# Performance work log

Hardware: AMD Instinct MI355X
Metric: run time of the kernel (lower is better)

The kernel has to match this reference:

```python
import jax, jax.numpy as jnp
import numpy as np
import math

B, H, S, D = 2, 16, 2048, 128

def setup_inputs() -> dict:
    key = jax.random.key(0)
    kq, kk, kv = jax.random.split(key, 3)
    return {
        "query": jax.random.normal(kq, (B, H, S, D), dtype=jnp.float32),
        "key": jax.random.normal(kk, (B, H, S, D), dtype=jnp.float32),
        "value": jax.random.normal(kv, (B, H, S, D), dtype=jnp.float32),
        "mask": jnp.ones((1, 1, S, S), dtype=jnp.bool_),
    }

def reference(query, key, value, mask):
    # scale_factor=None -> 1/sqrt(head_dim), as in standard SDPA
    head_dim = query.shape[-1]
    scale = 1.0 / math.sqrt(head_dim)
    # [B,H,Sq,Sk] attention scores
    scores = jnp.einsum("bhqd,bhkd->bhqk", query, key) * scale
    neg_inf = jnp.finfo(scores.dtype).min
    scores = jnp.where(mask, scores, neg_inf)
    attn = jax.nn.softmax(scores, axis=-1)  # dropout p=0.0 -> identity
    return jnp.einsum("bhqk,bhkd->bhqd", attn, value)
```

## Files before the change

kernel.cpp:

```cpp
#include <hip/hip_runtime.h>
#include <cstdint>

using short8  = __attribute__((ext_vector_type(8))) short;
using short2v = __attribute__((ext_vector_type(2))) short;
using f32x16  = __attribute__((ext_vector_type(16))) float;
using float4v = __attribute__((ext_vector_type(4))) float;
using int4v   = __attribute__((ext_vector_type(4))) int;

constexpr int Bc = 2, Hc = 16, Sc = 2048, Dc = 128;
constexpr int NW = 8, QBLK = 256;
constexpr int KVS = 128;
constexpr int NT = Sc / KVS;
constexpr float SCALE_LOG2E = 0.08838834764831845f * 1.4426950408889634f;

__device__ __forceinline__ short f2bf(float f) {
  union { float f; uint32_t u; } v; v.f = f;
  uint32_t u = v.u;
  uint32_t r = (u + 0x7FFFu + ((u >> 16) & 1u)) >> 16;
  return (short)r;
}

__device__ __forceinline__ uint32_t cvtpk(float lo, float hi) {
  uint32_t r;
  asm("v_cvt_pk_bf16_f32 %0, %1, %2" : "=v"(r) : "v"(lo), "v"(hi));
  return r;
}

#define GLOAD_LDS16(g, l)                                                     \
  __builtin_amdgcn_global_load_lds(                                           \
      (const __attribute__((address_space(1))) void*)(g),                     \
      (__attribute__((address_space(3))) void*)(l), 16, 0, 0)

__global__ __launch_bounds__(256)
void prep_v_kernel(const float* __restrict__ V, ushort* __restrict__ Vt) {
  __shared__ short T[64 * 66];
  const int bh = blockIdx.y;
  const int st = blockIdx.x & 31, dt = blockIdx.x >> 5;
  const int s0 = st * 64, d0 = dt * 64;
  const float* Vb = V + (size_t)bh * Sc * Dc;
  ushort* Vtb = Vt + (size_t)bh * Dc * Sc;
#pragma unroll
  for (int i = 0; i < 4; ++i) {
    int idx = threadIdx.x + i * 256;
    int r = idx >> 4, c4 = (idx & 15) * 4;
    float4v v = *(const float4v*)&Vb[(size_t)(s0 + r) * Dc + d0 + c4];
    short2v lo, hi;
    lo[0] = f2bf(v[0]); lo[1] = f2bf(v[1]);
    hi[0] = f2bf(v[2]); hi[1] = f2bf(v[3]);
    *(short2v*)&T[r * 66 + c4]     = lo;
    *(short2v*)&T[r * 66 + c4 + 2] = hi;
  }
  __syncthreads();
#pragma unroll
  for (int i = 0; i < 2; ++i) {
    int idx = threadIdx.x + i * 256;
    int dr = idx >> 3, c8 = (idx & 7) * 8;
    short8 o;
#pragma unroll
    for (int j = 0; j < 8; ++j) o[j] = T[(c8 + j) * 66 + dr];
    *(short8*)&Vtb[(size_t)(d0 + dr) * Sc + s0 + c8] = o;
  }
}

__global__ __launch_bounds__(512, 2)
void sdpa_fwd_kernel(const float* __restrict__ Q, const float* __restrict__ Kf,
                     const ushort* __restrict__ Vt, float* __restrict__ O) {
  __shared__ __align__(16) short Kl[2][KVS * Dc];
  __shared__ __align__(16) short Vl[2][Dc * KVS];

  const int tid  = threadIdx.x;
  const int w    = tid >> 6;
  const int lane = tid & 63;
  const int l31  = lane & 31;
  const int hi   = lane >> 5;

  const int bh = blockIdx.x & 31;
  const int qt = blockIdx.x >> 5;
  const size_t base = (size_t)bh * Sc * Dc;
  const float* Qb = Q + base;
  const float* KfB = Kf + base;
  const ushort* VtB = Vt + base;

  const int qrow = qt * QBLK + w * 32 + l31;

  short8 qf[8];
#pragma unroll
  for (int c = 0; c < 8; ++c) {
    const float* src = Qb + (size_t)qrow * Dc + c * 16 + hi * 8;
    float4v a = *(const float4v*)src;
    float4v b = *(const float4v*)(src + 4);
    short8 r;
    r[0] = f2bf(a[0] * SCALE_LOG2E); r[1] = f2bf(a[1] * SCALE_LOG2E);
    r[2] = f2bf(a[2] * SCALE_LOG2E); r[3] = f2bf(a[3] * SCALE_LOG2E);
    r[4] = f2bf(b[0] * SCALE_LOG2E); r[5] = f2bf(b[1] * SCALE_LOG2E);
    r[6] = f2bf(b[2] * SCALE_LOG2E); r[7] = f2bf(b[3] * SCALE_LOG2E);
    qf[c] = r;
  }

  int offK[4], kdst[4], offV[4], vldsOff[4];
#pragma unroll
  for (int j = 0; j < 4; ++j) {
    int row = w * 16 + j * 4 + (lane >> 4);
    offK[j] = row * Dc + (((lane & 15) ^ (row & 15)) * 8);
    kdst[j] = (w * 16 + j * 4) * Dc + lane * 8;
    int d = w * 16 + j * 4 + (lane >> 4);
    offV[j] = d * Sc + (((lane & 15) ^ (d & 15)) * 8);
    vldsOff[j] = (w * 16 + j * 4) * KVS;
  }

  float4v krA[4], krB[4];
  auto LOADK = [&](int kv0) {
#pragma unroll
    for (int j = 0; j < 4; ++j) {
      const float* s = KfB + (size_t)kv0 * Dc + offK[j];
      krA[j] = *(const float4v*)s;
      krB[j] = *(const float4v*)(s + 4);
    }
  };
  auto WRITEK = [&](int buf) {
#pragma unroll
    for (int j = 0; j < 4; ++j) {
      int4v kw;
      kw[0] = (int)cvtpk(krA[j][0], krA[j][1]);
      kw[1] = (int)cvtpk(krA[j][2], krA[j][3]);
      kw[2] = (int)cvtpk(krB[j][0], krB[j][1]);
      kw[3] = (int)cvtpk(krB[j][2], krB[j][3]);
      *(int4v*)&Kl[buf][kdst[j]] = kw;
    }
  };
  auto STAGEV = [&](int buf, int kv0) {
#pragma unroll
    for (int j = 0; j < 4; ++j)
      GLOAD_LDS16(VtB + kv0 + offV[j], &Vl[buf][vldsOff[j]]);
  };

  f32x16 acc[4];
#pragma unroll
  for (int i = 0; i < 4; ++i)
#pragma unroll
    for (int r = 0; r < 16; ++r) acc[i][r] = 0.f;
  float m_run = -1e30f, l_run = 0.f;

  LOADK(0);
  WRITEK(0);
  STAGEV(0, 0);
  LOADK(KVS);
  int cur = 0;

  for (int it = 0; it < NT; ++it) {
    __syncthreads();
    if (it + 1 < NT) { WRITEK(cur ^ 1); STAGEV(cur ^ 1, (it + 1) * KVS); }
    if (it + 2 < NT) LOADK((it + 2) * KVS);

#pragma unroll
    for (int sub = 0; sub < 2; ++sub) {
      f32x16 st0, st1;
#pragma unroll
      for (int r = 0; r < 16; ++r) { st0[r] = 0.f; st1[r] = 0.f; }
      __builtin_amdgcn_s_setprio(1);
#pragma unroll
      for (int c = 0; c < 8; ++c) {
        int e0 = ((sub * 64 + l31) * Dc + c * 16 + hi * 8) ^ ((l31 & 15) << 3);
        int e1 = ((sub * 64 + 32 + l31) * Dc + c * 16 + hi * 8) ^ ((l31 & 15) << 3);
        short8 kf0 = *(const short8*)&Kl[cur][e0];
        short8 kf1 = *(const short8*)&Kl[cur][e1];
        st0 = __builtin_amdgcn_mfma_f32_32x32x16_bf16(kf0, qf[c], st0, 0, 0, 0);
        st1 = __builtin_amdgcn_mfma_f32_32x32x16_bf16(kf1, qf[c], st1, 0, 0, 0);
      }
      __builtin_amdgcn_s_setprio(0);

      float t0 = st0[0], t1 = st0[1], t2 = st0[2], t3 = st0[3];
#pragma unroll
      for (int r = 4; r < 16; r += 4) {
        t0 = fmaxf(t0, st0[r]);     t1 = fmaxf(t1, st0[r + 1]);
        t2 = fmaxf(t2, st0[r + 2]); t3 = fmaxf(t3, st0[r + 3]);
      }
#pragma unroll
      for (int r = 0; r < 16; r += 4) {
        t0 = fmaxf(t0, st1[r]);     t1 = fmaxf(t1, st1[r + 1]);
        t2 = fmaxf(t2, st1[r + 2]); t3 = fmaxf(t3, st1[r + 3]);
      }
      float tmax = fmaxf(fmaxf(t0, t1), fmaxf(t2, t3));
      tmax = fmaxf(tmax, __shfl_xor(tmax, 32));

      if (!__all(tmax <= m_run + 8.0f)) {
        float m_new = fmaxf(m_run, tmax);
        float alpha = __builtin_amdgcn_exp2f(m_run - m_new);
        l_run *= alpha;
#pragma unroll
        for (int i = 0; i < 4; ++i)
#pragma unroll
          for (int r = 0; r < 16; ++r) acc[i][r] *= alpha;
        m_run = m_new;
      }

      float ps0 = 0.f, ps1 = 0.f, ps2 = 0.f, ps3 = 0.f;
#pragma unroll
      for (int r = 0; r < 16; r += 4) {
        float p0 = __builtin_amdgcn_exp2f(st0[r]     - m_run);
        float p1 = __builtin_amdgcn_exp2f(st0[r + 1] - m_run);
        float p2 = __builtin_amdgcn_exp2f(st0[r + 2] - m_run);
        float p3 = __builtin_amdgcn_exp2f(st0[r + 3] - m_run);
        st0[r] = p0; st0[r + 1] = p1; st0[r + 2] = p2; st0[r + 3] = p3;
        ps0 += p0; ps1 += p1; ps2 += p2; ps3 += p3;
      }
#pragma unroll
      for (int r = 0; r < 16; r += 4) {
        float p0 = __builtin_amdgcn_exp2f(st1[r]     - m_run);
        float p1 = __builtin_amdgcn_exp2f(st1[r + 1] - m_run);
        float p2 = __builtin_amdgcn_exp2f(st1[r + 2] - m_run);
        float p3 = __builtin_amdgcn_exp2f(st1[r + 3] - m_run);
        st1[r] = p0; st1[r + 1] = p1; st1[r + 2] = p2; st1[r + 3] = p3;
        ps0 += p0; ps1 += p1; ps2 += p2; ps3 += p3;
      }
      float psum = (ps0 + ps1) + (ps2 + ps3);
      psum += __shfl_xor(psum, 32);
      l_run += psum;

      short8 pf[4];
#pragma unroll
      for (int kc = 0; kc < 4; ++kc) {
        const f32x16& stq = (kc < 2) ? st0 : st1;
        const int g0 = (2 * kc) & 3, g1 = (2 * kc + 1) & 3;
        uint32_t a0 = cvtpk(stq[4 * g0 + 0], stq[4 * g0 + 1]);
        uint32_t b0 = cvtpk(stq[4 * g1 + 0], stq[4 * g1 + 1]);
        asm volatile("v_permlane32_swap_b32 %0, %1" : "+v"(a0), "+v"(b0));
        uint32_t a1 = cvtpk(stq[4 * g0 + 2], stq[4 * g0 + 3]);
        uint32_t b1 = cvtpk(stq[4 * g1 + 2], stq[4 * g1 + 3]);
        asm volatile("v_permlane32_swap_b32 %0, %1" : "+v"(a1), "+v"(b1));
        int4v wv; wv[0] = (int)a0; wv[1] = (int)a1; wv[2] = (int)b0; wv[3] = (int)b1;
        union { int4v i; short8 s; } u; u.i = wv;
        pf[kc] = u.s;
      }

      __builtin_amdgcn_s_setprio(1);
#pragma unroll
      for (int kc = 0; kc < 4; ++kc) {
#pragma unroll
        for (int dt = 0; dt < 4; ++dt) {
          int d = dt * 32 + l31;
          int elem = (d * KVS + sub * 64 + kc * 16 + hi * 8) ^ ((l31 & 15) << 3);
          short8 vf = *(const short8*)&Vl[cur][elem];
          acc[dt] = __builtin_amdgcn_mfma_f32_32x32x16_bf16(vf, pf[kc], acc[dt], 0, 0, 0);
        }
      }
      __builtin_amdgcn_s_setprio(0);
    }
    cur ^= 1;
  }

  const float inv_l = 1.0f / l_run;
  float* Ob = O + base + (size_t)qrow * Dc;
#pragma unroll
  for (int dt = 0; dt < 4; ++dt)
#pragma unroll
    for (int g = 0; g < 4; ++g) {
      float4v o;
      o[0] = acc[dt][4 * g + 0] * inv_l; o[1] = acc[dt][4 * g + 1] * inv_l;
      o[2] = acc[dt][4 * g + 2] * inv_l; o[3] = acc[dt][4 * g + 3] * inv_l;
      *(float4v*)&Ob[dt * 32 + 8 * g + 4 * hi] = o;
    }
}

extern "C" void kernel_launch(void* const* d_in, const int* in_sizes, int n_in,
                              void* d_out, int out_size, void* d_ws, size_t ws_size,
                              hipStream_t stream) {
  const float* Q = (const float*)d_in[0];
  const float* K = (const float*)d_in[1];
  const float* V = (const float*)d_in[2];
  float* O = (float*)d_out;

  ushort* Vt = (ushort*)d_ws;

  prep_v_kernel<<<dim3(64, Bc * Hc), dim3(256), 0, stream>>>(V, Vt);

  sdpa_fwd_kernel<<<dim3((Sc / QBLK) * Bc * Hc), dim3(512), 0, stream>>>(Q, K, Vt, O);
}
```

Measured before the change: 94.44 us.

## Fuse V bf16 conversion and transpose into attention kernel, drop prep kernel

Removes the separate kernel that converted V to bf16 and transposed it into workspace. Each attention block now loads fp32 V rows into registers, converts them, and scatters them transposed into swizzled LDS alongside the K pipeline. This removes a launch and a workspace round trip. In exchange it reads fp32 V once per query tile, adds many scalar 16-bit LDS stores per tile, and raises register pressure.

```diff
diff --git a/kernel.cpp b/kernel.cpp
--- a/kernel.cpp
+++ b/kernel.cpp
@@ -2,7 +2,6 @@
 #include <cstdint>
 
 using short8  = __attribute__((ext_vector_type(8))) short;
-using short2v = __attribute__((ext_vector_type(2))) short;
 using f32x16  = __attribute__((ext_vector_type(16))) float;
 using float4v = __attribute__((ext_vector_type(4))) float;
 using int4v   = __attribute__((ext_vector_type(4))) int;
@@ -26,45 +25,9 @@
   return r;
 }
 
-#define GLOAD_LDS16(g, l)                                                     \
-  __builtin_amdgcn_global_load_lds(                                           \
-      (const __attribute__((address_space(1))) void*)(g),                     \
-      (__attribute__((address_space(3))) void*)(l), 16, 0, 0)
-
-__global__ __launch_bounds__(256)
-void prep_v_kernel(const float* __restrict__ V, ushort* __restrict__ Vt) {
-  __shared__ short T[64 * 66];
-  const int bh = blockIdx.y;
-  const int st = blockIdx.x & 31, dt = blockIdx.x >> 5;
-  const int s0 = st * 64, d0 = dt * 64;
-  const float* Vb = V + (size_t)bh * Sc * Dc;
-  ushort* Vtb = Vt + (size_t)bh * Dc * Sc;
-#pragma unroll
-  for (int i = 0; i < 4; ++i) {
-    int idx = threadIdx.x + i * 256;
-    int r = idx >> 4, c4 = (idx & 15) * 4;
-    float4v v = *(const float4v*)&Vb[(size_t)(s0 + r) * Dc + d0 + c4];
-    short2v lo, hi;
-    lo[0] = f2bf(v[0]); lo[1] = f2bf(v[1]);
-    hi[0] = f2bf(v[2]); hi[1] = f2bf(v[3]);
-    *(short2v*)&T[r * 66 + c4]     = lo;
-    *(short2v*)&T[r * 66 + c4 + 2] = hi;
-  }
-  __syncthreads();
-#pragma unroll
-  for (int i = 0; i < 2; ++i) {
-    int idx = threadIdx.x + i * 256;
-    int dr = idx >> 3, c8 = (idx & 7) * 8;
-    short8 o;
-#pragma unroll
-    for (int j = 0; j < 8; ++j) o[j] = T[(c8 + j) * 66 + dr];
-    *(short8*)&Vtb[(size_t)(d0 + dr) * Sc + s0 + c8] = o;
-  }
-}
-
 __global__ __launch_bounds__(512, 2)
 void sdpa_fwd_kernel(const float* __restrict__ Q, const float* __restrict__ Kf,
-                     const ushort* __restrict__ Vt, float* __restrict__ O) {
+                     const float* __restrict__ Vf, float* __restrict__ O) {
   __shared__ __align__(16) short Kl[2][KVS * Dc];
   __shared__ __align__(16) short Vl[2][Dc * KVS];
 
@@ -79,7 +42,7 @@
   const size_t base = (size_t)bh * Sc * Dc;
   const float* Qb = Q + base;
   const float* KfB = Kf + base;
-  const ushort* VtB = Vt + base;
+  const float* VfB = Vf + base;
 
   const int qrow = qt * QBLK + w * 32 + l31;
 
@@ -97,15 +60,12 @@
     qf[c] = r;
   }
 
-  int offK[4], kdst[4], offV[4], vldsOff[4];
+  int offK[4], kdst[4];
 #pragma unroll
   for (int j = 0; j < 4; ++j) {
     int row = w * 16 + j * 4 + (lane >> 4);
     offK[j] = row * Dc + (((lane & 15) ^ (row & 15)) * 8);
     kdst[j] = (w * 16 + j * 4) * Dc + lane * 8;
-    int d = w * 16 + j * 4 + (lane >> 4);
-    offV[j] = d * Sc + (((lane & 15) ^ (d & 15)) * 8);
-    vldsOff[j] = (w * 16 + j * 4) * KVS;
   }
 
   float4v krA[4], krB[4];
@@ -128,10 +88,30 @@
       *(int4v*)&Kl[buf][kdst[j]] = kw;
     }
   };
-  auto STAGEV = [&](int buf, int kv0) {
-#pragma unroll
-    for (int j = 0; j < 4; ++j)
-      GLOAD_LDS16(VtB + kv0 + offV[j], &Vl[buf][vldsOff[j]]);
+
+  const int kvp = lane & 15, dp = lane >> 4;
+  const int kvv = w * 16 + kvp;
+  float4v vrA[4], vrB[4];
+  auto LOADV = [&](int kv0) {
+#pragma unroll
+    for (int j = 0; j < 4; ++j) {
+      const float* s = VfB + (size_t)(kv0 + kvv) * Dc + j * 32 + dp * 8;
+      vrA[j] = *(const float4v*)s;
+      vrB[j] = *(const float4v*)(s + 4);
+    }
+  };
+  auto WRITEV = [&](int buf) {
+    short* vl = &Vl[buf][0];
+#pragma unroll
+    for (int j = 0; j < 4; ++j) {
+#pragma unroll
+      for (int e = 0; e < 8; ++e) {
+        int dd = j * 32 + dp * 8 + e;
+        int flat = (dd * KVS + kvv) ^ ((dd & 15) << 3);
+        float x = (e < 4) ? vrA[j][e & 3] : vrB[j][e & 3];
+        vl[flat] = f2bf(x);
+      }
+    }
   };
 
   f32x16 acc[4];
@@ -141,16 +121,15 @@
     for (int r = 0; r < 16; ++r) acc[i][r] = 0.f;
   float m_run = -1e30f, l_run = 0.f;
 
-  LOADK(0);
-  WRITEK(0);
-  STAGEV(0, 0);
-  LOADK(KVS);
+  LOADK(0); LOADV(0);
+  WRITEK(0); WRITEV(0);
+  LOADK(KVS); LOADV(KVS);
   int cur = 0;
 
   for (int it = 0; it < NT; ++it) {
     __syncthreads();
-    if (it + 1 < NT) { WRITEK(cur ^ 1); STAGEV(cur ^ 1, (it + 1) * KVS); }
-    if (it + 2 < NT) LOADK((it + 2) * KVS);
+    if (it + 1 < NT) { WRITEK(cur ^ 1); WRITEV(cur ^ 1); }
+    if (it + 2 < NT) { LOADK((it + 2) * KVS); LOADV((it + 2) * KVS); }
 
 #pragma unroll
     for (int sub = 0; sub < 2; ++sub) {
@@ -270,9 +249,5 @@
   const float* V = (const float*)d_in[2];
   float* O = (float*)d_out;
 
-  ushort* Vt = (ushort*)d_ws;
-
-  prep_v_kernel<<<dim3(64, Bc * Hc), dim3(256), 0, stream>>>(V, Vt);
-
-  sdpa_fwd_kernel<<<dim3((Sc / QBLK) * Bc * Hc), dim3(512), 0, stream>>>(Q, K, Vt, O);
-}
+  sdpa_fwd_kernel<<<dim3((Sc / QBLK) * Bc * Hc), dim3(512), 0, stream>>>(Q, K, V, O);
+}
```

Measured after the change: 243.5 us. 2.58x slower.
